# Kernel tuning notes

Hardware: AMD Instinct MI355X
Metric: run time of the kernel (lower is better)

## Reference

```python
import jax, jax.numpy as jnp
import numpy as np
from jax import lax

B, S, H, A = 8, 2048, 16, 128   # batch, seq, num_head, i_head_dim
D = 128                          # o_head_dim
LN_EPS = 1e-6


def setup_inputs() -> dict:
    key = jax.random.key(0)
    ks = jax.random.split(key, 6)
    heads_input = jax.random.normal(ks[0], (B, S, H, A), dtype=jnp.float32)
    # grouped linear weights: (heads, in_per_head, out_per_head)
    w_hid = jax.random.normal(ks[1], (H, 2 * A, 3 * D), dtype=jnp.float32) * 0.02
    b_hid = jnp.zeros((H, 3 * D), dtype=jnp.float32)
    w_og = jax.random.normal(ks[2], (H, A + D, D), dtype=jnp.float32) * 0.02
    b_og = jnp.zeros((H, D), dtype=jnp.float32)
    ln_g = jnp.ones((H, A), dtype=jnp.float32)
    ln_b = jnp.zeros((H, A), dtype=jnp.float32)
    init_cx = jnp.zeros((H, D), dtype=jnp.float32)
    return {"heads_input": heads_input, "w_hid": w_hid, "b_hid": b_hid,
            "w_og": w_og, "b_og": b_og, "ln_g": ln_g, "ln_b": ln_b,
            "init_cx": init_cx}


def _ln2d(x, g, b):
    # LayerNorm over the last two dims (H, A)
    m = jnp.mean(x, axis=(-2, -1), keepdims=True)
    v = jnp.var(x, axis=(-2, -1), keepdims=True)
    return (x - m) * lax.rsqrt(v + LN_EPS) * g + b


def _forward(heads_input, w_hid, b_hid, w_og, b_og, ln_g, ln_b, init_cx):
    # cumulative-sum + LayerNorm (RS1cumsumstatnorm, states=None)
    csum = _ln2d(jnp.cumsum(heads_input, axis=1), ln_g, ln_b)  # (B,S,H,A)
    # grouped (per-head) linear: 2A -> 3D
    hid_in = jnp.concatenate([heads_input, csum], axis=-1)     # (B,S,H,2A)
    gates = jnp.einsum('bshi,hio->bsho', hid_in, w_hid) + b_hid  # (B,S,H,3D)
    igate, fgate, hidden = jnp.split(gates, 3, axis=-1)
    fgate = jax.nn.sigmoid(fgate)
    hidden = jax.nn.relu(hidden)
    igh = jax.nn.sigmoid(igate) * hidden                        # (B,S,H,D)
    # forget-gated linear recurrence c_t = f_t * c_{t-1} + igh_t (LGateFunc)
    def combine(c1, c2):
        a1, u1 = c1
        a2, u2 = c2
        return a1 * a2, u1 * a2 + u2
    F, C = lax.associative_scan(combine, (fgate, igh), axis=1)
    cell = C + F * init_cx[None, None]                          # (B,S,H,D)
    # output gate: grouped linear (A+D -> D), sigmoid, gate the cell
    og_in = jnp.concatenate([heads_input, cell], axis=-1)       # (B,S,H,A+D)
    og = jax.nn.sigmoid(jnp.einsum('bshi,hio->bsho', og_in, w_og) + b_og)
    return og * cell


def reference(heads_input, w_hid, b_hid, w_og, b_og, ln_g, ln_b, init_cx):
    return _forward(heads_input, w_hid, b_hid, w_og, b_og, ln_g, ln_b, init_cx)
```

## Files before the change

### kernel.cpp

```cpp
#include <hip/hip_runtime.h>
#include <stdint.h>

#define Bb 8
#define Ss 2048
#define Hh 16
#define Aa 128
#define Dd 128
#define NGATE 384
#define KDIM 256
#define NCH 16
#define CLEN 128
#define ROWS (Bb*Ss)
#define ROWSTR (Hh*Aa)

typedef float f32x4 __attribute__((ext_vector_type(4)));
typedef __bf16 bf16x8 __attribute__((ext_vector_type(8)));
typedef unsigned short u16x8 __attribute__((ext_vector_type(8)));

static __device__ __forceinline__ unsigned short f2bf(float f){
  unsigned int u = __builtin_bit_cast(unsigned int, f);
  u += 0x7FFFu + ((u >> 16) & 1u);
  return (unsigned short)(u >> 16);
}
static __device__ __forceinline__ float bf2f(unsigned short s){
  unsigned int u = ((unsigned int)s) << 16;
  return __builtin_bit_cast(float, u);
}
static __device__ __forceinline__ float sigf(float x){ return 1.0f/(1.0f + __expf(-x)); }

__global__ void k_conv_whid(const float* __restrict__ w, unsigned short* __restrict__ wt){
  int idx = blockIdx.x*256 + threadIdx.x;
  const int total = Hh*KDIM*NGATE;
  for (; idx < total; idx += gridDim.x*256){
    int o = idx % NGATE; int k = (idx/NGATE) % KDIM; int h = idx/(NGATE*KDIM);
    int g = o >> 7, d = o & 127;
    int nh = d >> 6, dl = d & 63;
    int wn = dl >> 4, ln15 = d & 15;
    int ks = k >> 5, lq = (k >> 3) & 3, kb = k & 7;
    int hy = h*2 + nh;
    int l = lq*16 + ln15;
    size_t dst = (size_t)hy*(192*KDIM) + (size_t)((((wn*8 + ks)*3 + g)*64 + l)*8 + kb);
    wt[dst] = f2bf(w[idx]);
  }
}
__global__ void k_conv_wog(const float* __restrict__ w, unsigned short* __restrict__ wt){
  int idx = blockIdx.x*256 + threadIdx.x;
  const int total = Hh*KDIM*Dd;
  for (; idx < total; idx += gridDim.x*256){
    int o = idx % Dd; int k = (idx/Dd) % KDIM; int h = idx/(Dd*KDIM);
    wt[(size_t)h*(Dd*KDIM) + o*KDIM + k] = f2bf(w[idx]);
  }
}

__global__ void k_cumsum_a(const float* __restrict__ x, float* __restrict__ totals){
  int c = blockIdx.x;
  int k = c % NCH; int hb = c / NCH;
  int b = hb / Hh, h = hb % Hh;
  int a = threadIdx.x;
  const float* p = x + ((size_t)(b*Ss + k*CLEN)*Hh + h)*Aa + a;
  float run = 0.f;
  #pragma unroll 4
  for (int i = 0; i < CLEN; ++i) run += p[(size_t)i*ROWSTR];
  totals[(size_t)c*Aa + a] = run;
}

__global__ void k_cumsum_c(const float* __restrict__ x, const float* __restrict__ totals,
                           unsigned short* __restrict__ csum, unsigned short* __restrict__ xbf){
  int c = blockIdx.x;
  int k = c % NCH; int hb = c / NCH;
  int b = hb / Hh, h = hb % Hh;
  int a = threadIdx.x;
  const float* tp = totals + (size_t)hb*NCH*Aa + a;
  float run = 0.f;
  for (int j = 0; j < k; ++j) run += tp[(size_t)j*Aa];
  const size_t base = ((size_t)(b*Ss + k*CLEN)*Hh + h)*Aa + a;
  const float* p = x + base;
  unsigned short* q  = csum + base;
  unsigned short* xq = xbf  + base;
  #pragma unroll 2
  for (int i = 0; i < CLEN; ++i){
    float v = p[(size_t)i*ROWSTR];
    run += v;
    q [(size_t)i*ROWSTR] = f2bf(run);
    xq[(size_t)i*ROWSTR] = f2bf(v);
  }
}

__global__ void k_stats(const unsigned short* __restrict__ csum, float2* __restrict__ mr){
  int r = blockIdx.x;
  int t = threadIdx.x;
  const u16x8 v = *(const u16x8*)(csum + (size_t)r*ROWSTR + t*8);
  float s = 0.f, q = 0.f;
  #pragma unroll
  for (int i = 0; i < 8; ++i){ float f = bf2f(v[i]); s += f; q += f*f; }
  #pragma unroll
  for (int off = 32; off; off >>= 1){ s += __shfl_down(s, off); q += __shfl_down(q, off); }
  __shared__ float ls[4], lq[4];
  int wid = t >> 6, lane = t & 63;
  if (lane == 0){ ls[wid] = s; lq[wid] = q; }
  __syncthreads();
  if (t == 0){
    float S2 = ls[0]+ls[1]+ls[2]+ls[3], Q = lq[0]+lq[1]+lq[2]+lq[3];
    float mu = S2 * (1.0f/(float)ROWSTR);
    float var = Q * (1.0f/(float)ROWSTR) - mu*mu;
    mr[r] = make_float2(mu, rsqrtf(var + 1e-6f));
  }
}

#define GSRC(kk_) (((kk_) < 2) ? xbf : csum)
#define GCO(kk_)  (((kk_) & 1) * 64)
#define GROWT(t_) ((mg*16 + (t_))*128)
__launch_bounds__(512, 2)
__global__ void k_gates(const unsigned short* __restrict__ xbf,
                        const unsigned short* __restrict__ csum,
                        const float2* __restrict__ mr,
                        const float* __restrict__ ln_g, const float* __restrict__ ln_b,
                        const unsigned short* __restrict__ wht,
                        const float* __restrict__ b_hid, unsigned int* __restrict__ fu){
  __shared__ unsigned short lA[2][128*64];
  const int mg = blockIdx.x, hy = blockIdx.y;
  const int h = hy >> 1, nh = hy & 1;
  const int tid = threadIdx.x;
  const int lane = tid & 63, wid = tid >> 6;
  const int wm = wid & 1, wn = wid >> 1;
  const int ln15 = lane & 15, lq = lane >> 4;
  const int r0 = tid >> 3, q0 = tid & 7;
  const int lwA0 = (r0*128 + q0*16) ^ ((r0 & 7) << 4);
  const int lwA1 = ((r0+64)*128 + q0*16) ^ ((r0 & 7) << 4);

  bf16x8 Bf[8][3];
  {
    const u16x8* bs8 = (const u16x8*)(wht + (size_t)hy*(192*KDIM));
    #pragma unroll
    for (int ks = 0; ks < 8; ++ks)
      #pragma unroll
      for (int g = 0; g < 3; ++g)
        Bf[ks][g] = __builtin_bit_cast(bf16x8, bs8[((wn*8 + ks)*3 + g)*64 + lane]);
  }
  const int dcol = nh*64 + wn*16 + ln15;
  const float big = b_hid[h*NGATE + dcol];
  const float bfg = b_hid[h*NGATE + 128 + dcol];
  const float bhd = b_hid[h*NGATE + 256 + dcol];

  f32x4 acc[4][3];
  #pragma unroll
  for (int i = 0; i < 4; ++i)
    #pragma unroll
    for (int j = 0; j < 3; ++j) acc[i][j] = (f32x4){0.f,0.f,0.f,0.f};

  u16x8 pa0, pa1;

#define GA_FETCH(t_, kk_) do { \
    const unsigned short* as_ = GSRC(kk_); \
    const size_t base_ = (size_t)(GROWT(t_) + r0)*ROWSTR + h*Aa + GCO(kk_) + q0*8; \
    pa0 = *(const u16x8*)(as_ + base_); \
    pa1 = *(const u16x8*)(as_ + base_ + (size_t)64*ROWSTR); \
  } while(0)
#define GA_WRITE(t_, kk_, buf_) do { \
    if ((kk_) >= 2){ \
      float2 m0_ = mr[GROWT(t_) + r0]; \
      float2 m1_ = mr[GROWT(t_) + r0 + 64]; \
      const float* g_  = ln_g + h*Aa + GCO(kk_) + q0*8; \
      const float* bz_ = ln_b + h*Aa + GCO(kk_) + q0*8; \
      u16x8 o0_, o1_; \
      _Pragma("unroll") \
      for (int i_ = 0; i_ < 8; ++i_){ \
        float gg_ = g_[i_], bb_ = bz_[i_]; \
        o0_[i_] = f2bf((bf2f(pa0[i_]) - m0_.x)*m0_.y*gg_ + bb_); \
        o1_[i_] = f2bf((bf2f(pa1[i_]) - m1_.x)*m1_.y*gg_ + bb_); \
      } \
      *(u16x8*)((char*)lA[buf_] + lwA0) = o0_; \
      *(u16x8*)((char*)lA[buf_] + lwA1) = o1_; \
    } else { \
      *(u16x8*)((char*)lA[buf_] + lwA0) = pa0; \
      *(u16x8*)((char*)lA[buf_] + lwA1) = pa1; \
    } \
  } while(0)

  GA_FETCH(0, 0); GA_WRITE(0, 0, 0);
  GA_FETCH(0, 1);

  for (int t = 0; t < 16; ++t){
    #pragma unroll
    for (int kk = 0; kk < 4; ++kk){
      const int cur = kk & 1;
      __syncthreads();
      if (kk < 3){
        GA_WRITE(t, kk+1, cur^1);
        if (kk + 2 < 4) GA_FETCH(t, kk+2);
        else if (t + 1 < 16) GA_FETCH(t+1, 0);
      } else {
        if (t + 1 < 16){
          GA_WRITE(t+1, 0, cur^1);
          GA_FETCH(t+1, 1);
        }
      }
      #pragma unroll
      for (int ks2 = 0; ks2 < 2; ++ks2){
        const int kel = ks2*32 + lq*8;
        bf16x8 af[4];
        #pragma unroll
        for (int mf = 0; mf < 4; ++mf){
          int ra = wm*64 + mf*16 + ln15;
          af[mf] = __builtin_bit_cast(bf16x8,
            *(const u16x8*)((const char*)lA[cur] + ((ra*128 + kel*2) ^ ((ra & 7) << 4))));
        }
        #pragma unroll
        for (int g = 0; g < 3; ++g)
          #pragma unroll
          for (int mf = 0; mf < 4; ++mf)
            acc[mf][g] = __builtin_amdgcn_mfma_f32_16x16x32_bf16(
                af[mf], Bf[kk*2 + ks2][g], acc[mf][g], 0, 0, 0);
      }
      if (kk == 3){
        const int m0 = GROWT(t);
        #pragma unroll
        for (int mf = 0; mf < 4; ++mf){
          const int rowb = m0 + wm*64 + mf*16 + lq*4;
          f32x4 aig = acc[mf][0], afg = acc[mf][1], ahd = acc[mf][2];
          #pragma unroll
          for (int r = 0; r < 4; ++r){
            float fg = sigf(afg[r] + bfg);
            float uu = sigf(aig[r] + big) * fmaxf(ahd[r] + bhd, 0.0f);
            fu[(size_t)(rowb + r)*ROWSTR + h*Dd + dcol] =
              ((unsigned int)f2bf(uu) << 16) | (unsigned int)f2bf(fg);
          }
          acc[mf][0] = (f32x4){0.f,0.f,0.f,0.f};
          acc[mf][1] = (f32x4){0.f,0.f,0.f,0.f};
          acc[mf][2] = (f32x4){0.f,0.f,0.f,0.f};
        }
      }
    }
  }
#undef GA_FETCH
#undef GA_WRITE
}

__global__ void k_recur_a(const unsigned int* __restrict__ fu,
                          float* __restrict__ Fc, float* __restrict__ Cc){
  int c = blockIdx.x;
  int k = c % NCH; int hb = c / NCH;
  int b = hb / Hh, h = hb % Hh;
  int d = threadIdx.x;
  const unsigned int* p = fu + ((size_t)(b*Ss + k*CLEN)*Hh + h)*Dd + d;
  float F = 1.f, C = 0.f;
  #pragma unroll 4
  for (int i = 0; i < CLEN; ++i){
    unsigned int v = p[(size_t)i*ROWSTR];
    float f = bf2f((unsigned short)v);
    float u = bf2f((unsigned short)(v >> 16));
    C = fmaf(f, C, u);
    F *= f;
  }
  Fc[(size_t)c*Dd + d] = F;
  Cc[(size_t)c*Dd + d] = C;
}

__global__ void k_recur_b(const float* __restrict__ Fc, const float* __restrict__ Cc,
                          const float* __restrict__ init_cx, float* __restrict__ gcarry){
  int bh = blockIdx.x;
  int h = bh % Hh;
  int d = threadIdx.x;
  float carry = init_cx[h*Dd + d];
  for (int j = 0; j < NCH; ++j){
    size_t o = ((size_t)bh*NCH + j)*Dd + d;
    gcarry[o] = carry;
    carry = fmaf(Fc[o], carry, Cc[o]);
  }
}

#define CPITCH 132
#define XPITCH 136
__launch_bounds__(512, 2)
__global__ void k_og_fused(const unsigned short* __restrict__ xbf,
                           const unsigned int* __restrict__ fu,
                           const unsigned short* __restrict__ wot,
                           const float* __restrict__ gcarry,
                           const float* __restrict__ b_og, float* __restrict__ out){
  __shared__ float s_cell[128*CPITCH];
  __shared__ unsigned short s_xa[128*XPITCH];
  __shared__ float2 s_scan[4*128];
  __shared__ float s_cc[128];
  const int mg = blockIdx.x;
  const int h  = blockIdx.y;
  const int tid = threadIdx.x;
  const int lane = tid & 63, wid = tid >> 6;
  const int wm = wid >> 2, wn = wid & 3;
  const int ln15 = lane & 15, lq = lane >> 4;
  const int rd = tid & 127, rq = tid >> 7;

  bf16x8 Bf[8][2];
  {
    unsigned short* bst = (unsigned short*)s_cell;
    const u16x8* bs = (const u16x8*)(wot + (size_t)h*(Dd*KDIM));
    u16x8* d8 = (u16x8*)bst;
    #pragma unroll
    for (int i = 0; i < 8; ++i) d8[tid + i*512] = bs[tid + i*512];
    if (tid < 128)
      s_cc[tid] = gcarry[((size_t)((mg>>1)*Hh + h)*NCH + (mg & 1)*8)*Dd + tid];
    __syncthreads();
    #pragma unroll
    for (int ks = 0; ks < 8; ++ks)
      #pragma unroll
      for (int j = 0; j < 2; ++j){
        int n = wn*32 + j*16 + ln15;
        Bf[ks][j] = __builtin_bit_cast(bf16x8,
          *(const u16x8*)(bst + n*KDIM + ks*32 + lq*8));
      }
    __syncthreads();
  }

  f32x4 acc[4][2];
  #pragma unroll
  for (int i = 0; i < 4; ++i){ acc[i][0] = (f32x4){0,0,0,0}; acc[i][1] = (f32x4){0,0,0,0}; }

  for (int t = 0; t < 8; ++t){
    const int row0 = (mg*8 + t)*128;
    unsigned int uf[32];
    const unsigned int* fp = fu + (size_t)(row0 + rq*32)*ROWSTR + h*Dd + rd;
    #pragma unroll
    for (int i = 0; i < 32; ++i) uf[i] = fp[(size_t)i*ROWSTR];
    #pragma unroll
    for (int i = 0; i < 4; ++i){
      int c = tid + i*512;
      int r = c >> 4, c8 = c & 15;
      u16x8 v = *(const u16x8*)(xbf + (size_t)(row0 + r)*ROWSTR + h*Aa + c8*8);
      *(u16x8*)&s_xa[r*XPITCH + c8*8] = v;
    }
    float F = 1.f, C = 0.f;
    #pragma unroll
    for (int i = 0; i < 32; ++i){
      float f = bf2f((unsigned short)uf[i]);
      float u = bf2f((unsigned short)(uf[i] >> 16));
      C = fmaf(f, C, u); F *= f;
    }
    s_scan[rq*128 + rd] = make_float2(F, C);
    __syncthreads();
    float cin = s_cc[rd];
    #pragma unroll
    for (int qq = 0; qq < 3; ++qq){
      if (rq > qq){ float2 s = s_scan[qq*128 + rd]; cin = fmaf(s.x, cin, s.y); }
    }
    __syncthreads();
    if (rq == 3){ float2 s3 = s_scan[3*128 + rd]; s_cc[rd] = fmaf(s3.x, cin, s3.y); }
    {
      float c = cin;
      #pragma unroll
      for (int i = 0; i < 32; ++i){
        float f = bf2f((unsigned short)uf[i]);
        float u = bf2f((unsigned short)(uf[i] >> 16));
        c = fmaf(f, c, u);
        s_cell[(rq*32 + i)*CPITCH + rd] = c;
      }
    }
    __syncthreads();
    #pragma unroll
    for (int ks = 0; ks < 4; ++ks){
      bf16x8 af[4];
      #pragma unroll
      for (int mf = 0; mf < 4; ++mf){
        int ra = wm*64 + mf*16 + ln15;
        af[mf] = __builtin_bit_cast(bf16x8,
          *(const u16x8*)&s_xa[ra*XPITCH + ks*32 + lq*8]);
      }
      #pragma unroll
      for (int mf = 0; mf < 4; ++mf)
        #pragma unroll
        for (int j = 0; j < 2; ++j)
          acc[mf][j] = __builtin_amdgcn_mfma_f32_16x16x32_bf16(af[mf], Bf[ks][j], acc[mf][j], 0, 0, 0);
    }
    #pragma unroll
    for (int ks = 4; ks < 8; ++ks){
      bf16x8 af[4];
      #pragma unroll
      for (int mf = 0; mf < 4; ++mf){
        int ra = wm*64 + mf*16 + ln15;
        const float* cp = &s_cell[ra*CPITCH + (ks-4)*32 + lq*8];
        f32x4 c0 = *(const f32x4*)cp;
        f32x4 c1 = *(const f32x4*)(cp + 4);
        u16x8 tt;
        tt[0]=f2bf(c0[0]); tt[1]=f2bf(c0[1]); tt[2]=f2bf(c0[2]); tt[3]=f2bf(c0[3]);
        tt[4]=f2bf(c1[0]); tt[5]=f2bf(c1[1]); tt[6]=f2bf(c1[2]); tt[7]=f2bf(c1[3]);
        af[mf] = __builtin_bit_cast(bf16x8, tt);
      }
      #pragma unroll
      for (int mf = 0; mf < 4; ++mf)
        #pragma unroll
        for (int j = 0; j < 2; ++j)
          acc[mf][j] = __builtin_amdgcn_mfma_f32_16x16x32_bf16(af[mf], Bf[ks][j], acc[mf][j], 0, 0, 0);
    }
    #pragma unroll
    for (int mf = 0; mf < 4; ++mf){
      const int rl = wm*64 + mf*16 + lq*4;
      #pragma unroll
      for (int j = 0; j < 2; ++j){
        const int d = wn*32 + j*16 + ln15;
        const float bo = b_og[h*Dd + d];
        #pragma unroll
        for (int r = 0; r < 4; ++r){
          float cell = s_cell[(rl + r)*CPITCH + d];
          out[(size_t)(row0 + rl + r)*ROWSTR + h*Dd + d] = sigf(acc[mf][j][r] + bo) * cell;
        }
        acc[mf][j] = (f32x4){0.f,0.f,0.f,0.f};
      }
    }
    __syncthreads();
  }
}

extern "C" void kernel_launch(void* const* d_in, const int* in_sizes, int n_in,
                              void* d_out, int out_size, void* d_ws, size_t ws_size,
                              hipStream_t stream){
  const float* x       = (const float*)d_in[0];
  const float* w_hid   = (const float*)d_in[1];
  const float* b_hid   = (const float*)d_in[2];
  const float* w_og    = (const float*)d_in[3];
  const float* b_og    = (const float*)d_in[4];
  const float* ln_g    = (const float*)d_in[5];
  const float* ln_b    = (const float*)d_in[6];
  const float* init_cx = (const float*)d_in[7];
  float* out = (float*)d_out;

  char* ws = (char*)d_ws;
  unsigned short* csum = (unsigned short*)(ws);
  unsigned int*   fu   = (unsigned int*)  (ws + ((size_t)64  << 20));
  unsigned short* xbf  = (unsigned short*)(ws + ((size_t)192 << 20));
  float*          tot  = (float*)         (ws + ((size_t)256 << 20));
  float*          Fc   = (float*)         (ws + ((size_t)257 << 20));
  float*          Cc   = (float*)         (ws + ((size_t)258 << 20));
  float2*         mr   = (float2*)        (ws + ((size_t)259 << 20));
  unsigned short* wht  = (unsigned short*)(ws + ((size_t)260 << 20));
  unsigned short* wot  = (unsigned short*)(ws + ((size_t)263 << 20));
  float*          gcar = (float*)         (ws + ((size_t)264 << 20));

  k_conv_whid<<<2048, 256, 0, stream>>>(w_hid, wht);
  k_conv_wog <<<1024, 256, 0, stream>>>(w_og,  wot);
  k_cumsum_a <<<Bb*Hh*NCH, Aa, 0, stream>>>(x, tot);
  k_cumsum_c <<<Bb*Hh*NCH, Aa, 0, stream>>>(x, tot, csum, xbf);
  k_stats    <<<ROWS, 256, 0, stream>>>(csum, mr);
  k_gates    <<<dim3(8, 32), 512, 0, stream>>>(xbf, csum, mr, ln_g, ln_b, wht, b_hid, fu);
  k_recur_a  <<<Bb*Hh*NCH, Dd, 0, stream>>>(fu, Fc, Cc);
  k_recur_b  <<<Bb*Hh, Dd, 0, stream>>>(Fc, Cc, init_cx, gcar);
  k_og_fused <<<dim3(16, 16), 512, 0, stream>>>(xbf, fu, wot, gcar, b_og, out);
}
```

Baseline: 342.3 us.

## Fold LayerNorm affine into gate weights and apply row stats in epilogue

LayerNorm's gain is folded into the csum half of the gate weights, and the mean/bias terms go into precomputed per-head vectors. The gates GEMM then feeds raw bf16 cumsum values straight to the MFMA and keeps separate accumulators for the x and csum parts. The per-row rstd and mean correction is applied in the epilogue, which removes the per-element normalize-and-convert work from the LDS staging path. The cost is doubled accumulator registers and a new small precompute kernel. Precision may change because raw cumsum values, with large magnitudes, are rounded to bf16 before normalization.

```diff
diff --git a/kernel.cpp b/kernel.cpp
--- a/kernel.cpp
+++ b/kernel.cpp
@@ -28,7 +28,8 @@
 }
 static __device__ __forceinline__ float sigf(float x){ return 1.0f/(1.0f + __expf(-x)); }
 
-__global__ void k_conv_whid(const float* __restrict__ w, unsigned short* __restrict__ wt){
+__global__ void k_conv_whid(const float* __restrict__ w, const float* __restrict__ ln_g,
+                            unsigned short* __restrict__ wt){
   int idx = blockIdx.x*256 + threadIdx.x;
   const int total = Hh*KDIM*NGATE;
   for (; idx < total; idx += gridDim.x*256){
@@ -39,8 +40,10 @@
     int ks = k >> 5, lq = (k >> 3) & 3, kb = k & 7;
     int hy = h*2 + nh;
     int l = lq*16 + ln15;
+    float wv = w[idx];
+    if (k >= 128) wv *= ln_g[h*Aa + (k - 128)];
     size_t dst = (size_t)hy*(192*KDIM) + (size_t)((((wn*8 + ks)*3 + g)*64 + l)*8 + kb);
-    wt[dst] = f2bf(w[idx]);
+    wt[dst] = f2bf(wv);
   }
 }
 __global__ void k_conv_wog(const float* __restrict__ w, unsigned short* __restrict__ wt){
@@ -50,6 +53,24 @@
     int o = idx % Dd; int k = (idx/Dd) % KDIM; int h = idx/(Dd*KDIM);
     wt[(size_t)h*(Dd*KDIM) + o*KDIM + k] = f2bf(w[idx]);
   }
+}
+
+__global__ void k_wext(const float* __restrict__ w, const float* __restrict__ b_hid,
+                       const float* __restrict__ ln_g, const float* __restrict__ ln_b,
+                       float* __restrict__ W1, float* __restrict__ b2){
+  int h = blockIdx.x;
+  int o = threadIdx.x;
+  float s1 = 0.f, s2 = 0.f;
+  const float* wp = w + ((size_t)h*KDIM + 128)*NGATE + o;
+  const float* gp = ln_g + h*Aa;
+  const float* bp = ln_b + h*Aa;
+  for (int a = 0; a < 128; ++a){
+    float wv = wp[(size_t)a*NGATE];
+    s1 = fmaf(wv, gp[a], s1);
+    s2 = fmaf(wv, bp[a], s2);
+  }
+  W1[h*NGATE + o] = s1;
+  b2[h*NGATE + o] = b_hid[h*NGATE + o] + s2;
 }
 
 __global__ void k_cumsum_a(const float* __restrict__ x, float* __restrict__ totals){
@@ -114,9 +135,9 @@
 __global__ void k_gates(const unsigned short* __restrict__ xbf,
                         const unsigned short* __restrict__ csum,
                         const float2* __restrict__ mr,
-                        const float* __restrict__ ln_g, const float* __restrict__ ln_b,
                         const unsigned short* __restrict__ wht,
-                        const float* __restrict__ b_hid, unsigned int* __restrict__ fu){
+                        const float* __restrict__ W1t, const float* __restrict__ b2t,
+                        unsigned int* __restrict__ fu){
   __shared__ unsigned short lA[2][128*64];
   const int mg = blockIdx.x, hy = blockIdx.y;
   const int h = hy >> 1, nh = hy & 1;
@@ -138,46 +159,33 @@
         Bf[ks][g] = __builtin_bit_cast(bf16x8, bs8[((wn*8 + ks)*3 + g)*64 + lane]);
   }
   const int dcol = nh*64 + wn*16 + ln15;
-  const float big = b_hid[h*NGATE + dcol];
-  const float bfg = b_hid[h*NGATE + 128 + dcol];
-  const float bhd = b_hid[h*NGATE + 256 + dcol];
-
-  f32x4 acc[4][3];
+  const float W1ig = W1t[h*NGATE + dcol];
+  const float W1fg = W1t[h*NGATE + 128 + dcol];
+  const float W1hd = W1t[h*NGATE + 256 + dcol];
+  const float b2ig = b2t[h*NGATE + dcol];
+  const float b2fg = b2t[h*NGATE + 128 + dcol];
+  const float b2hd = b2t[h*NGATE + 256 + dcol];
+
+  f32x4 aX[4][3], aC[4][3];
   #pragma unroll
   for (int i = 0; i < 4; ++i)
     #pragma unroll
-    for (int j = 0; j < 3; ++j) acc[i][j] = (f32x4){0.f,0.f,0.f,0.f};
+    for (int j = 0; j < 3; ++j){ aX[i][j] = (f32x4){0.f,0.f,0.f,0.f}; aC[i][j] = (f32x4){0.f,0.f,0.f,0.f}; }
 
   u16x8 pa0, pa1;
 
 #define GA_FETCH(t_, kk_) do { \
     const unsigned short* as_ = GSRC(kk_); \
-    const size_t base_ = (size_t)(GROWT(t_) + r0)*ROWSTR + h*Aa + GCO(kk_) + q0*8; \
+    const unsigned base_ = ((unsigned)(GROWT(t_) + r0) << 11) + h*Aa + GCO(kk_) + q0*8; \
     pa0 = *(const u16x8*)(as_ + base_); \
-    pa1 = *(const u16x8*)(as_ + base_ + (size_t)64*ROWSTR); \
+    pa1 = *(const u16x8*)(as_ + base_ + (64u << 11)); \
   } while(0)
-#define GA_WRITE(t_, kk_, buf_) do { \
-    if ((kk_) >= 2){ \
-      float2 m0_ = mr[GROWT(t_) + r0]; \
-      float2 m1_ = mr[GROWT(t_) + r0 + 64]; \
-      const float* g_  = ln_g + h*Aa + GCO(kk_) + q0*8; \
-      const float* bz_ = ln_b + h*Aa + GCO(kk_) + q0*8; \
-      u16x8 o0_, o1_; \
-      _Pragma("unroll") \
-      for (int i_ = 0; i_ < 8; ++i_){ \
-        float gg_ = g_[i_], bb_ = bz_[i_]; \
-        o0_[i_] = f2bf((bf2f(pa0[i_]) - m0_.x)*m0_.y*gg_ + bb_); \
-        o1_[i_] = f2bf((bf2f(pa1[i_]) - m1_.x)*m1_.y*gg_ + bb_); \
-      } \
-      *(u16x8*)((char*)lA[buf_] + lwA0) = o0_; \
-      *(u16x8*)((char*)lA[buf_] + lwA1) = o1_; \
-    } else { \
-      *(u16x8*)((char*)lA[buf_] + lwA0) = pa0; \
-      *(u16x8*)((char*)lA[buf_] + lwA1) = pa1; \
-    } \
+#define GA_WRITE(buf_) do { \
+    *(u16x8*)((char*)lA[buf_] + lwA0) = pa0; \
+    *(u16x8*)((char*)lA[buf_] + lwA1) = pa1; \
   } while(0)
 
-  GA_FETCH(0, 0); GA_WRITE(0, 0, 0);
+  GA_FETCH(0, 0); GA_WRITE(0);
   GA_FETCH(0, 1);
 
   for (int t = 0; t < 16; ++t){
@@ -186,14 +194,12 @@
       const int cur = kk & 1;
       __syncthreads();
       if (kk < 3){
-        GA_WRITE(t, kk+1, cur^1);
+        GA_WRITE(cur^1);
         if (kk + 2 < 4) GA_FETCH(t, kk+2);
         else if (t + 1 < 16) GA_FETCH(t+1, 0);
-      } else {
-        if (t + 1 < 16){
-          GA_WRITE(t+1, 0, cur^1);
-          GA_FETCH(t+1, 1);
-        }
+      } else if (t + 1 < 16){
+        GA_WRITE(cur^1);
+        GA_FETCH(t+1, 1);
       }
       #pragma unroll
       for (int ks2 = 0; ks2 < 2; ++ks2){
@@ -208,26 +214,37 @@
         #pragma unroll
         for (int g = 0; g < 3; ++g)
           #pragma unroll
-          for (int mf = 0; mf < 4; ++mf)
-            acc[mf][g] = __builtin_amdgcn_mfma_f32_16x16x32_bf16(
-                af[mf], Bf[kk*2 + ks2][g], acc[mf][g], 0, 0, 0);
+          for (int mf = 0; mf < 4; ++mf){
+            if (kk < 2)
+              aX[mf][g] = __builtin_amdgcn_mfma_f32_16x16x32_bf16(
+                  af[mf], Bf[kk*2 + ks2][g], aX[mf][g], 0, 0, 0);
+            else
+              aC[mf][g] = __builtin_amdgcn_mfma_f32_16x16x32_bf16(
+                  af[mf], Bf[kk*2 + ks2][g], aC[mf][g], 0, 0, 0);
+          }
       }
       if (kk == 3){
         const int m0 = GROWT(t);
         #pragma unroll
         for (int mf = 0; mf < 4; ++mf){
           const int rowb = m0 + wm*64 + mf*16 + lq*4;
-          f32x4 aig = acc[mf][0], afg = acc[mf][1], ahd = acc[mf][2];
           #pragma unroll
           for (int r = 0; r < 4; ++r){
-            float fg = sigf(afg[r] + bfg);
-            float uu = sigf(aig[r] + big) * fmaxf(ahd[r] + bhd, 0.0f);
-            fu[(size_t)(rowb + r)*ROWSTR + h*Dd + dcol] =
+            float2 m = mr[rowb + r];
+            float rs = m.y, mm = m.x * m.y;
+            float pig = aX[mf][0][r] + rs*aC[mf][0][r] - mm*W1ig + b2ig;
+            float pfg = aX[mf][1][r] + rs*aC[mf][1][r] - mm*W1fg + b2fg;
+            float phd = aX[mf][2][r] + rs*aC[mf][2][r] - mm*W1hd + b2hd;
+            float fg = sigf(pfg);
+            float uu = sigf(pig) * fmaxf(phd, 0.0f);
+            fu[((unsigned)(rowb + r) << 11) + h*Dd + dcol] =
               ((unsigned int)f2bf(uu) << 16) | (unsigned int)f2bf(fg);
           }
-          acc[mf][0] = (f32x4){0.f,0.f,0.f,0.f};
-          acc[mf][1] = (f32x4){0.f,0.f,0.f,0.f};
-          acc[mf][2] = (f32x4){0.f,0.f,0.f,0.f};
+          #pragma unroll
+          for (int g = 0; g < 3; ++g){
+            aX[mf][g] = (f32x4){0.f,0.f,0.f,0.f};
+            aC[mf][g] = (f32x4){0.f,0.f,0.f,0.f};
+          }
         }
       }
     }
@@ -429,16 +446,19 @@
   float*          Fc   = (float*)         (ws + ((size_t)257 << 20));
   float*          Cc   = (float*)         (ws + ((size_t)258 << 20));
   float2*         mr   = (float2*)        (ws + ((size_t)259 << 20));
+  float*          W1   = (float*)         (ws + ((size_t)259 << 20) + (128u << 10));
+  float*          b2   = (float*)         (ws + ((size_t)259 << 20) + (160u << 10));
   unsigned short* wht  = (unsigned short*)(ws + ((size_t)260 << 20));
   unsigned short* wot  = (unsigned short*)(ws + ((size_t)263 << 20));
   float*          gcar = (float*)         (ws + ((size_t)264 << 20));
 
-  k_conv_whid<<<2048, 256, 0, stream>>>(w_hid, wht);
+  k_conv_whid<<<2048, 256, 0, stream>>>(w_hid, ln_g, wht);
   k_conv_wog <<<1024, 256, 0, stream>>>(w_og,  wot);
+  k_wext     <<<Hh, NGATE, 0, stream>>>(w_hid, b_hid, ln_g, ln_b, W1, b2);
   k_cumsum_a <<<Bb*Hh*NCH, Aa, 0, stream>>>(x, tot);
   k_cumsum_c <<<Bb*Hh*NCH, Aa, 0, stream>>>(x, tot, csum, xbf);
   k_stats    <<<ROWS, 256, 0, stream>>>(csum, mr);
-  k_gates    <<<dim3(8, 32), 512, 0, stream>>>(xbf, csum, mr, ln_g, ln_b, wht, b_hid, fu);
+  k_gates    <<<dim3(8, 32), 512, 0, stream>>>(xbf, csum, mr, wht, W1, b2, fu);
   k_recur_a  <<<Bb*Hh*NCH, Dd, 0, stream>>>(fu, Fc, Cc);
   k_recur_b  <<<Bb*Hh, Dd, 0, stream>>>(Fc, Cc, init_cx, gcar);
   k_og_fused <<<dim3(16, 16), 512, 0, stream>>>(xbf, fu, wot, gcar, b_og, out);
```

Result: slower. 380.1 us (+11.1%).
